# Kernel optimization log

Measured on AMD Instinct MI355X. Metric: run time of the kernel, lower is better.

Reference implementation:

```python
import jax, jax.numpy as jnp
import numpy as np

NEG_SLOPE = 0.2
EPS = 1e-16

N_NODES = 100000
N_EDGES = 1600000
CHANNELS = 128
M_LAYERS = 3


def setup_inputs() -> dict:
    key = jax.random.key(0)
    k1, k2, k3, k4, k5 = jax.random.split(key, 5)
    x = jax.random.normal(k1, (N_NODES, CHANNELS), dtype=jnp.float32)
    edge_index = jax.random.randint(k2, (2, N_EDGES), 0, N_NODES, dtype=jnp.int64)
    # Glorot-ish scaled params, stacked over layers
    Ws = jax.random.normal(k3, (M_LAYERS, CHANNELS, CHANNELS), dtype=jnp.float32) / np.sqrt(CHANNELS)
    att_src = jax.random.normal(k4, (M_LAYERS, CHANNELS), dtype=jnp.float32) / np.sqrt(CHANNELS)
    att_dst = jax.random.normal(k5, (M_LAYERS, CHANNELS), dtype=jnp.float32) / np.sqrt(CHANNELS)
    bias = jnp.zeros((M_LAYERS, CHANNELS), dtype=jnp.float32)
    return {"x": x, "edge_index": edge_index, "Ws": Ws, "att_src": att_src,
            "att_dst": att_dst, "bias": bias}


def _gat_conv(x, src, dst, W, a_src, a_dst, b, n_nodes):
    # single-head PyG GATConv (heads=1, concat) with self-loops already in src/dst
    h = x @ W                                   # [N, C]
    s = h @ a_src                               # [N] per-node source score
    d = h @ a_dst                               # [N] per-node dest score
    e = s[src] + d[dst]                         # [E]
    e = jnp.where(e > 0, e, NEG_SLOPE * e)      # LeakyReLU(0.2)
    # segment softmax over edges grouped by destination node
    e_max = jax.ops.segment_max(e, dst, num_segments=n_nodes)
    e_max = jnp.where(jnp.isfinite(e_max), e_max, 0.0)
    w = jnp.exp(e - e_max[dst])                 # [E]
    denom = jax.ops.segment_sum(w, dst, num_segments=n_nodes)
    alpha = w / (denom[dst] + EPS)              # [E]
    out = jax.ops.segment_sum(alpha[:, None] * h[src], dst, num_segments=n_nodes)
    return out + b


def reference(x, edge_index, Ws, att_src, att_dst, bias):
    n = x.shape[0]
    loop = jnp.arange(n, dtype=edge_index.dtype)
    src = jnp.concatenate([edge_index[0], loop])   # add self loops (PyG default)
    dst = jnp.concatenate([edge_index[1], loop])
    for m in range(Ws.shape[0]):
        x = x + jax.nn.sigmoid(
            _gat_conv(x, src, dst, Ws[m], att_src[m], att_dst[m], bias[m], n))
    return x
```

## Files before the change

kernel.cpp:

```cpp
#include <hip/hip_runtime.h>
#include <hip/hip_bf16.h>
#include <math.h>

#define CH 128
#define LAYERS 3
#define NEG_SLOPE 0.2f
#define EPS_D 1e-16f
#define NBUCK_MAX 512
#define BIN_CHUNK 8192
#define PAIR_STRIDE 4608

typedef __attribute__((ext_vector_type(8))) short bf16x8;
typedef __attribute__((ext_vector_type(4))) short s16x4;
typedef __attribute__((ext_vector_type(4))) float f32x4;
typedef __attribute__((ext_vector_type(2))) float f32x2;

__device__ __forceinline__ float leaky(float e) { return e > 0.f ? e : NEG_SLOPE * e; }
__device__ __forceinline__ float sigm(float x) { return 1.f / (1.f + __expf(-x)); }

__device__ __forceinline__ unsigned bf16rne(float f) {
    unsigned u = __float_as_uint(f);
    return (u + 0x7fffu + ((u >> 16) & 1u)) >> 16;
}
__device__ __forceinline__ unsigned pack2(float f0, float f1) {
    return bf16rne(f0) | (bf16rne(f1) << 16);
}

__global__ __launch_bounds__(256) void bin_k(const int* __restrict__ EI,
                                             int* __restrict__ bcursor,
                                             unsigned* __restrict__ pairs,
                                             int ne, int nbuck) {
    __shared__ int hist[NBUCK_MAX];
    __shared__ int base[NBUCK_MAX];
    const int t = threadIdx.x;
    const int e0 = blockIdx.x * BIN_CHUNK;
    const int e1 = min(e0 + BIN_CHUNK, ne);

    for (int i = t; i < nbuck; i += 256) hist[i] = 0;
    __syncthreads();
    for (int e = e0 + t; e < e1; e += 256)
        atomicAdd(&hist[EI[ne + e] >> 8], 1);
    __syncthreads();
    for (int i = t; i < nbuck; i += 256) {
        int c = hist[i];
        base[i] = (c > 0) ? (i * PAIR_STRIDE + atomicAdd(&bcursor[i], c)) : 0;
        hist[i] = 0;
    }
    __syncthreads();
    for (int e = e0 + t; e < e1; e += 256) {
        int src = EI[e], dst = EI[ne + e];
        int b = dst >> 8;
        int off = atomicAdd(&hist[b], 1);
        pairs[base[b] + off] = ((unsigned)src << 8) | (unsigned)(dst & 255);
    }
}

__global__ __launch_bounds__(256) void bscat_k(const int* __restrict__ bcursor,
                                               const unsigned* __restrict__ pairs,
                                               int* __restrict__ col,
                                               int* __restrict__ rowbeg,
                                               int* __restrict__ rowend, int n) {
    __shared__ int hist[256];
    __shared__ int cur[256];
    __shared__ int wsum[4];
    const int b = blockIdx.x;
    const int node0 = b << 8;
    const int t = threadIdx.x;
    const int lane = t & 63, w = t >> 6;

    hist[t] = 0;
    __syncthreads();
    const int pbase = b * PAIR_STRIDE;
    const int tot = bcursor[b];
    for (int i = t; i < tot; i += 256)
        atomicAdd(&hist[pairs[pbase + i] & 255u], 1);
    __syncthreads();

    int v = hist[t];
    int sc = v;
#pragma unroll
    for (int off = 1; off < 64; off <<= 1) {
        int x = __shfl_up(sc, off);
        if (lane >= off) sc += x;
    }
    if (lane == 63) wsum[w] = sc;
    __syncthreads();
    if (t == 0) {
        int a = 0;
#pragma unroll
        for (int j = 0; j < 4; j++) { int tmp = wsum[j]; wsum[j] = a; a += tmp; }
    }
    __syncthreads();
    int excl = sc - v + wsum[w];
    int node = node0 + t;
    int rp = pbase + excl;
    if (node < n) {
        rowbeg[node] = rp;
        rowend[node] = rp + v;
        cur[t] = rp;
    }
    __syncthreads();

    for (int i = t; i < tot; i += 256) {
        unsigned p = pairs[pbase + i];
        int pos = atomicAdd(&cur[p & 255u], 1);
        col[pos] = (int)(p >> 8);
    }
}

__global__ __launch_bounds__(512) void gemm_k(const float* __restrict__ X,
                                              const float* __restrict__ Wm,
                                              const float* __restrict__ asrc,
                                              const float* __restrict__ adst,
                                              unsigned* __restrict__ Hf8,
                                              float* __restrict__ s,
                                              float* __restrict__ d, int n) {
    __shared__ short WT[128 * 132];
    const int t = threadIdx.x;
    const int node0 = blockIdx.x * 128;

    unsigned* WT32 = (unsigned*)WT;
#pragma unroll
    for (int i = 0; i < 16; i++) {
        int item = i * 512 + t;
        int c = item & 127, k2 = item >> 7;
        float va = Wm[(2 * k2) * 128 + c];
        float vb = Wm[(2 * k2 + 1) * 128 + c];
        WT32[c * 66 + k2] = pack2(va, vb);
    }
    __syncthreads();

    const int lane = t & 63, w = t >> 6;
    const int lr = lane & 15, lg = lane >> 4;
    const int row = w * 16 + lr;
    const int node = node0 + row;
    const int nodeA = min(node, n - 1);
    const float* xrow = X + (size_t)nodeA * CH;

    f32x4 acc[8];
#pragma unroll
    for (int ct = 0; ct < 8; ct++) acc[ct] = (f32x4){0.f, 0.f, 0.f, 0.f};

#pragma unroll
    for (int kt = 0; kt < 4; kt++) {
        const int kb = kt * 32 + lg * 8;
        const float4 fa = *(const float4*)&xrow[kb];
        const float4 fb = *(const float4*)&xrow[kb + 4];
        bf16x8 a;
        a[0] = (short)bf16rne(fa.x); a[1] = (short)bf16rne(fa.y);
        a[2] = (short)bf16rne(fa.z); a[3] = (short)bf16rne(fa.w);
        a[4] = (short)bf16rne(fb.x); a[5] = (short)bf16rne(fb.y);
        a[6] = (short)bf16rne(fb.z); a[7] = (short)bf16rne(fb.w);
#pragma unroll
        for (int ct = 0; ct < 8; ct++) {
            const int cc = ct * 16 + lr;
            s16x4 b0 = *(s16x4*)&WT[cc * 132 + kb];
            s16x4 b1 = *(s16x4*)&WT[cc * 132 + kb + 4];
            bf16x8 bb = {b0[0], b0[1], b0[2], b0[3], b1[0], b1[1], b1[2], b1[3]};
            acc[ct] = __builtin_amdgcn_mfma_f32_16x16x32_bf16(a, bb, acc[ct], 0, 0, 0);
        }
    }

    float asv[8], adv[8];
#pragma unroll
    for (int ct = 0; ct < 8; ct++) { asv[ct] = asrc[ct * 16 + lr]; adv[ct] = adst[ct * 16 + lr]; }

#pragma unroll
    for (int r = 0; r < 4; r++) {
        const int orow = w * 16 + lg * 4 + r;
        const int onode = node0 + orow;
        float ps = 0.f, pd = 0.f;
#pragma unroll
        for (int ct = 0; ct < 8; ct++) {
            float hv = acc[ct][r];
            ps += hv * asv[ct];
            pd += hv * adv[ct];
        }
        if (onode < n) {
            int w0 = __builtin_amdgcn_cvt_pk_fp8_f32(acc[0][r], acc[1][r], 0, false);
            w0 = __builtin_amdgcn_cvt_pk_fp8_f32(acc[2][r], acc[3][r], w0, true);
            int w1 = __builtin_amdgcn_cvt_pk_fp8_f32(acc[4][r], acc[5][r], 0, false);
            w1 = __builtin_amdgcn_cvt_pk_fp8_f32(acc[6][r], acc[7][r], w1, true);
            uint2 q8; q8.x = (unsigned)w0; q8.y = (unsigned)w1;
            *(uint2*)&Hf8[(size_t)onode * 32 + lr * 2] = q8;
        }
#pragma unroll
        for (int off = 8; off >= 1; off >>= 1) {
            ps += __shfl_xor(ps, off);
            pd += __shfl_xor(pd, off);
        }
        if (lr == 0 && onode < n) { s[onode] = ps; d[onode] = pd; }
    }
}

__global__ __launch_bounds__(256) void node_aggr_k(const int* __restrict__ rowbeg,
                                                   const int* __restrict__ rowend,
                                                   const int* __restrict__ col,
                                                   const float* __restrict__ s,
                                                   const float* __restrict__ d,
                                                   const unsigned* __restrict__ Hf8,
                                                   const float* __restrict__ bias,
                                                   const float* __restrict__ x_prev,
                                                   float* __restrict__ x_next, int n) {
    long g = (long)blockIdx.x * 256 + threadIdx.x;
    int node = (int)(g >> 4);
    if (node >= n) return;
    const int tid = threadIdx.x;
    const int sub = tid & 15;
    const int qbase = tid & 48;

    const int beg = rowbeg[node], end = rowend[node];
    const float dn = d[node];
    const float ev_self = leaky(s[node] + dn);

    float m = ev_self;
    float l = 0.f;
    float o[8];
#pragma unroll
    for (int k = 0; k < 8; k++) o[k] = 0.f;

    for (int j0 = beg; j0 < end; j0 += 16) {
        int cnt = min(16, end - j0);
        int srcv = 0;
        float ev = -INFINITY;
        if (sub < cnt) {
            srcv = col[j0 + sub];
            ev = leaky(s[srcv] + dn);
        }
        float bmax = ev;
#pragma unroll
        for (int off = 8; off >= 1; off >>= 1) bmax = fmaxf(bmax, __shfl_xor(bmax, off));
        float newm = fmaxf(m, bmax);
        float scale = __expf(m - newm);
        l *= scale;
#pragma unroll
        for (int k = 0; k < 8; k++) o[k] *= scale;
        m = newm;
        float wv = (sub < cnt) ? __expf(ev - m) : 0.f;

        for (int j = 0; j < cnt; j += 4) {
            int i1 = min(j + 1, cnt - 1), i2 = min(j + 2, cnt - 1), i3 = min(j + 3, cnt - 1);
            int se0 = __shfl(srcv, qbase + j);
            int se1 = __shfl(srcv, qbase + i1);
            int se2 = __shfl(srcv, qbase + i2);
            int se3 = __shfl(srcv, qbase + i3);
            float w0 = __shfl(wv, qbase + j);
            float w1 = __shfl(wv, qbase + i1);
            float w2 = __shfl(wv, qbase + i2);
            float w3 = __shfl(wv, qbase + i3);
            w1 = (j + 1 < cnt) ? w1 : 0.f;
            w2 = (j + 2 < cnt) ? w2 : 0.f;
            w3 = (j + 3 < cnt) ? w3 : 0.f;
            const uint2 u0 = *(const uint2*)&Hf8[(size_t)se0 * 32 + sub * 2];
            const uint2 u1 = *(const uint2*)&Hf8[(size_t)se1 * 32 + sub * 2];
            const uint2 u2 = *(const uint2*)&Hf8[(size_t)se2 * 32 + sub * 2];
            const uint2 u3 = *(const uint2*)&Hf8[(size_t)se3 * 32 + sub * 2];
            l += w0 + w1 + w2 + w3;
            {
                f32x2 p0 = __builtin_amdgcn_cvt_pk_f32_fp8(u0.x, false);
                f32x2 p1 = __builtin_amdgcn_cvt_pk_f32_fp8(u0.x, true);
                f32x2 p2 = __builtin_amdgcn_cvt_pk_f32_fp8(u0.y, false);
                f32x2 p3 = __builtin_amdgcn_cvt_pk_f32_fp8(u0.y, true);
                o[0] += w0 * p0[0]; o[1] += w0 * p0[1];
                o[2] += w0 * p1[0]; o[3] += w0 * p1[1];
                o[4] += w0 * p2[0]; o[5] += w0 * p2[1];
                o[6] += w0 * p3[0]; o[7] += w0 * p3[1];
            }
            {
                f32x2 p0 = __builtin_amdgcn_cvt_pk_f32_fp8(u1.x, false);
                f32x2 p1 = __builtin_amdgcn_cvt_pk_f32_fp8(u1.x, true);
                f32x2 p2 = __builtin_amdgcn_cvt_pk_f32_fp8(u1.y, false);
                f32x2 p3 = __builtin_amdgcn_cvt_pk_f32_fp8(u1.y, true);
                o[0] += w1 * p0[0]; o[1] += w1 * p0[1];
                o[2] += w1 * p1[0]; o[3] += w1 * p1[1];
                o[4] += w1 * p2[0]; o[5] += w1 * p2[1];
                o[6] += w1 * p3[0]; o[7] += w1 * p3[1];
            }
            {
                f32x2 p0 = __builtin_amdgcn_cvt_pk_f32_fp8(u2.x, false);
                f32x2 p1 = __builtin_amdgcn_cvt_pk_f32_fp8(u2.x, true);
                f32x2 p2 = __builtin_amdgcn_cvt_pk_f32_fp8(u2.y, false);
                f32x2 p3 = __builtin_amdgcn_cvt_pk_f32_fp8(u2.y, true);
                o[0] += w2 * p0[0]; o[1] += w2 * p0[1];
                o[2] += w2 * p1[0]; o[3] += w2 * p1[1];
                o[4] += w2 * p2[0]; o[5] += w2 * p2[1];
                o[6] += w2 * p3[0]; o[7] += w2 * p3[1];
            }
            {
                f32x2 p0 = __builtin_amdgcn_cvt_pk_f32_fp8(u3.x, false);
                f32x2 p1 = __builtin_amdgcn_cvt_pk_f32_fp8(u3.x, true);
                f32x2 p2 = __builtin_amdgcn_cvt_pk_f32_fp8(u3.y, false);
                f32x2 p3 = __builtin_amdgcn_cvt_pk_f32_fp8(u3.y, true);
                o[0] += w3 * p0[0]; o[1] += w3 * p0[1];
                o[2] += w3 * p1[0]; o[3] += w3 * p1[1];
                o[4] += w3 * p2[0]; o[5] += w3 * p2[1];
                o[6] += w3 * p3[0]; o[7] += w3 * p3[1];
            }
        }
    }

    float wself = __expf(ev_self - m);
    l += wself;
    const uint2 us = *(const uint2*)&Hf8[(size_t)node * 32 + sub * 2];
    {
        f32x2 p0 = __builtin_amdgcn_cvt_pk_f32_fp8(us.x, false);
        f32x2 p1 = __builtin_amdgcn_cvt_pk_f32_fp8(us.x, true);
        f32x2 p2 = __builtin_amdgcn_cvt_pk_f32_fp8(us.y, false);
        f32x2 p3 = __builtin_amdgcn_cvt_pk_f32_fp8(us.y, true);
        o[0] += wself * p0[0]; o[1] += wself * p0[1];
        o[2] += wself * p1[0]; o[3] += wself * p1[1];
        o[4] += wself * p2[0]; o[5] += wself * p2[1];
        o[6] += wself * p3[0]; o[7] += wself * p3[1];
    }

    float inv = 1.f / (l + EPS_D);
    const long rowb = (long)node * CH;
#pragma unroll
    for (int k = 0; k < 8; k++) {
        int c = k * 16 + sub;
        float r = x_prev[rowb + c] + sigm(o[k] * inv + bias[c]);
        x_next[rowb + c] = r;
    }
}

extern "C" void kernel_launch(void* const* d_in, const int* in_sizes, int n_in,
                              void* d_out, int out_size, void* d_ws, size_t ws_size,
                              hipStream_t stream) {
    const float* x_in = (const float*)d_in[0];
    const int* EI = (const int*)d_in[1];
    const float* Ws_all = (const float*)d_in[2];
    const float* asrc_all = (const float*)d_in[3];
    const float* adst_all = (const float*)d_in[4];
    const float* bias_all = (const float*)d_in[5];
    float* out = (float*)d_out;

    const int n = in_sizes[0] / CH;
    const int ne = in_sizes[1] / 2;
    const long NC = (long)n * CH;
    const int nbuck = (n + 255) >> 8;

    unsigned* hf8 = (unsigned*)d_ws;
    float* s = (float*)(hf8 + NC / 4);
    float* dd = s + n;
    float* x_ws = dd + n;
    int* rowbeg = (int*)(x_ws + NC);
    int* rowend = rowbeg + n;
    int* bcursor = rowend + n;
    int* colv = bcursor + nbuck;
    unsigned* pairs = (unsigned*)(colv + nbuck * PAIR_STRIDE);

    hipMemsetAsync(bcursor, 0, (size_t)nbuck * sizeof(int), stream);
    bin_k<<<(ne + BIN_CHUNK - 1) / BIN_CHUNK, 256, 0, stream>>>(EI, bcursor, pairs, ne, nbuck);
    bscat_k<<<nbuck, 256, 0, stream>>>(bcursor, pairs, colv, rowbeg, rowend, n);

    const float* xp[LAYERS] = {x_in, out, x_ws};
    float* xn[LAYERS] = {out, x_ws, out};

    for (int m = 0; m < LAYERS; m++) {
        const float* Wm = Ws_all + (size_t)m * CH * CH;
        const float* as = asrc_all + (size_t)m * CH;
        const float* ad = adst_all + (size_t)m * CH;
        const float* bm = bias_all + (size_t)m * CH;

        gemm_k<<<(n + 127) / 128, 512, 0, stream>>>(xp[m], Wm, as, ad, hf8, s, dd, n);
        node_aggr_k<<<((long)n * 16 + 255) / 256, 256, 0, stream>>>(rowbeg, rowend, colv,
                                                                    s, dd, hf8, bm,
                                                                    xp[m], xn[m], n);
    }
}
```

Measured before the change: 241.9 us.

## Store intermediate layer activations in bf16 and use packed f32x2 accumulation

Intermediate residual activations between layers are now written and read as bf16 rather than fp32, which halves that traffic in the gemm and aggregation kernels. The gemm can then load bf16 rows directly with no per-element conversion. The aggregation accumulator is rewritten to use f32x2 vectors so the compiler can emit packed FMA instructions. The cost is extra rounding error in the residual stream, which carries across layers.

```diff
diff --git a/kernel.cpp b/kernel.cpp
--- a/kernel.cpp
+++ b/kernel.cpp
@@ -24,6 +24,9 @@
 }
 __device__ __forceinline__ unsigned pack2(float f0, float f1) {
     return bf16rne(f0) | (bf16rne(f1) << 16);
+}
+__device__ __forceinline__ float bf16tof(unsigned short v) {
+    return __uint_as_float(((unsigned)v) << 16);
 }
 
 __global__ __launch_bounds__(256) void bin_k(const int* __restrict__ EI,
@@ -108,7 +111,8 @@
     }
 }
 
-__global__ __launch_bounds__(512) void gemm_k(const float* __restrict__ X,
+template <int XBF16>
+__global__ __launch_bounds__(512) void gemm_k(const void* __restrict__ Xv,
                                               const float* __restrict__ Wm,
                                               const float* __restrict__ asrc,
                                               const float* __restrict__ adst,
@@ -135,7 +139,6 @@
     const int row = w * 16 + lr;
     const int node = node0 + row;
     const int nodeA = min(node, n - 1);
-    const float* xrow = X + (size_t)nodeA * CH;
 
     f32x4 acc[8];
 #pragma unroll
@@ -144,13 +147,19 @@
 #pragma unroll
     for (int kt = 0; kt < 4; kt++) {
         const int kb = kt * 32 + lg * 8;
-        const float4 fa = *(const float4*)&xrow[kb];
-        const float4 fb = *(const float4*)&xrow[kb + 4];
         bf16x8 a;
-        a[0] = (short)bf16rne(fa.x); a[1] = (short)bf16rne(fa.y);
-        a[2] = (short)bf16rne(fa.z); a[3] = (short)bf16rne(fa.w);
-        a[4] = (short)bf16rne(fb.x); a[5] = (short)bf16rne(fb.y);
-        a[6] = (short)bf16rne(fb.z); a[7] = (short)bf16rne(fb.w);
+        if (XBF16) {
+            const unsigned short* xrow = (const unsigned short*)Xv + (size_t)nodeA * CH;
+            a = *(const bf16x8*)&xrow[kb];
+        } else {
+            const float* xrow = (const float*)Xv + (size_t)nodeA * CH;
+            const float4 fa = *(const float4*)&xrow[kb];
+            const float4 fb = *(const float4*)&xrow[kb + 4];
+            a[0] = (short)bf16rne(fa.x); a[1] = (short)bf16rne(fa.y);
+            a[2] = (short)bf16rne(fa.z); a[3] = (short)bf16rne(fa.w);
+            a[4] = (short)bf16rne(fb.x); a[5] = (short)bf16rne(fb.y);
+            a[6] = (short)bf16rne(fb.z); a[7] = (short)bf16rne(fb.w);
+        }
 #pragma unroll
         for (int ct = 0; ct < 8; ct++) {
             const int cc = ct * 16 + lr;
@@ -193,6 +202,15 @@
     }
 }
 
+__device__ __forceinline__ void acc_edge(f32x2* o2, const uint2 u, float we) {
+    f32x2 w2 = {we, we};
+    o2[0] += w2 * __builtin_amdgcn_cvt_pk_f32_fp8(u.x, false);
+    o2[1] += w2 * __builtin_amdgcn_cvt_pk_f32_fp8(u.x, true);
+    o2[2] += w2 * __builtin_amdgcn_cvt_pk_f32_fp8(u.y, false);
+    o2[3] += w2 * __builtin_amdgcn_cvt_pk_f32_fp8(u.y, true);
+}
+
+template <int PBF16, int NBF16>
 __global__ __launch_bounds__(256) void node_aggr_k(const int* __restrict__ rowbeg,
                                                    const int* __restrict__ rowend,
                                                    const int* __restrict__ col,
@@ -200,8 +218,8 @@
                                                    const float* __restrict__ d,
                                                    const unsigned* __restrict__ Hf8,
                                                    const float* __restrict__ bias,
-                                                   const float* __restrict__ x_prev,
-                                                   float* __restrict__ x_next, int n) {
+                                                   const void* __restrict__ x_prev,
+                                                   void* __restrict__ x_next, int n) {
     long g = (long)blockIdx.x * 256 + threadIdx.x;
     int node = (int)(g >> 4);
     if (node >= n) return;
@@ -215,9 +233,9 @@
 
     float m = ev_self;
     float l = 0.f;
-    float o[8];
-#pragma unroll
-    for (int k = 0; k < 8; k++) o[k] = 0.f;
+    f32x2 o2[4];
+#pragma unroll
+    for (int j = 0; j < 4; j++) o2[j] = (f32x2){0.f, 0.f};
 
     for (int j0 = beg; j0 < end; j0 += 16) {
         int cnt = min(16, end - j0);
@@ -232,9 +250,10 @@
         for (int off = 8; off >= 1; off >>= 1) bmax = fmaxf(bmax, __shfl_xor(bmax, off));
         float newm = fmaxf(m, bmax);
         float scale = __expf(m - newm);
+        f32x2 sc2 = {scale, scale};
         l *= scale;
 #pragma unroll
-        for (int k = 0; k < 8; k++) o[k] *= scale;
+        for (int j = 0; j < 4; j++) o2[j] *= sc2;
         m = newm;
         float wv = (sub < cnt) ? __expf(ev - m) : 0.f;
 
@@ -256,70 +275,31 @@
             const uint2 u2 = *(const uint2*)&Hf8[(size_t)se2 * 32 + sub * 2];
             const uint2 u3 = *(const uint2*)&Hf8[(size_t)se3 * 32 + sub * 2];
             l += w0 + w1 + w2 + w3;
-            {
-                f32x2 p0 = __builtin_amdgcn_cvt_pk_f32_fp8(u0.x, false);
-                f32x2 p1 = __builtin_amdgcn_cvt_pk_f32_fp8(u0.x, true);
-                f32x2 p2 = __builtin_amdgcn_cvt_pk_f32_fp8(u0.y, false);
-                f32x2 p3 = __builtin_amdgcn_cvt_pk_f32_fp8(u0.y, true);
-                o[0] += w0 * p0[0]; o[1] += w0 * p0[1];
-                o[2] += w0 * p1[0]; o[3] += w0 * p1[1];
-                o[4] += w0 * p2[0]; o[5] += w0 * p2[1];
-                o[6] += w0 * p3[0]; o[7] += w0 * p3[1];
-            }
-            {
-                f32x2 p0 = __builtin_amdgcn_cvt_pk_f32_fp8(u1.x, false);
-                f32x2 p1 = __builtin_amdgcn_cvt_pk_f32_fp8(u1.x, true);
-                f32x2 p2 = __builtin_amdgcn_cvt_pk_f32_fp8(u1.y, false);
-                f32x2 p3 = __builtin_amdgcn_cvt_pk_f32_fp8(u1.y, true);
-                o[0] += w1 * p0[0]; o[1] += w1 * p0[1];
-                o[2] += w1 * p1[0]; o[3] += w1 * p1[1];
-                o[4] += w1 * p2[0]; o[5] += w1 * p2[1];
-                o[6] += w1 * p3[0]; o[7] += w1 * p3[1];
-            }
-            {
-                f32x2 p0 = __builtin_amdgcn_cvt_pk_f32_fp8(u2.x, false);
-                f32x2 p1 = __builtin_amdgcn_cvt_pk_f32_fp8(u2.x, true);
-                f32x2 p2 = __builtin_amdgcn_cvt_pk_f32_fp8(u2.y, false);
-                f32x2 p3 = __builtin_amdgcn_cvt_pk_f32_fp8(u2.y, true);
-                o[0] += w2 * p0[0]; o[1] += w2 * p0[1];
-                o[2] += w2 * p1[0]; o[3] += w2 * p1[1];
-                o[4] += w2 * p2[0]; o[5] += w2 * p2[1];
-                o[6] += w2 * p3[0]; o[7] += w2 * p3[1];
-            }
-            {
-                f32x2 p0 = __builtin_amdgcn_cvt_pk_f32_fp8(u3.x, false);
-                f32x2 p1 = __builtin_amdgcn_cvt_pk_f32_fp8(u3.x, true);
-                f32x2 p2 = __builtin_amdgcn_cvt_pk_f32_fp8(u3.y, false);
-                f32x2 p3 = __builtin_amdgcn_cvt_pk_f32_fp8(u3.y, true);
-                o[0] += w3 * p0[0]; o[1] += w3 * p0[1];
-                o[2] += w3 * p1[0]; o[3] += w3 * p1[1];
-                o[4] += w3 * p2[0]; o[5] += w3 * p2[1];
-                o[6] += w3 * p3[0]; o[7] += w3 * p3[1];
-            }
+            acc_edge(o2, u0, w0);
+            acc_edge(o2, u1, w1);
+            acc_edge(o2, u2, w2);
+            acc_edge(o2, u3, w3);
         }
     }
 
     float wself = __expf(ev_self - m);
     l += wself;
     const uint2 us = *(const uint2*)&Hf8[(size_t)node * 32 + sub * 2];
-    {
-        f32x2 p0 = __builtin_amdgcn_cvt_pk_f32_fp8(us.x, false);
-        f32x2 p1 = __builtin_amdgcn_cvt_pk_f32_fp8(us.x, true);
-        f32x2 p2 = __builtin_amdgcn_cvt_pk_f32_fp8(us.y, false);
-        f32x2 p3 = __builtin_amdgcn_cvt_pk_f32_fp8(us.y, true);
-        o[0] += wself * p0[0]; o[1] += wself * p0[1];
-        o[2] += wself * p1[0]; o[3] += wself * p1[1];
-        o[4] += wself * p2[0]; o[5] += wself * p2[1];
-        o[6] += wself * p3[0]; o[7] += wself * p3[1];
-    }
+    acc_edge(o2, us, wself);
 
     float inv = 1.f / (l + EPS_D);
     const long rowb = (long)node * CH;
 #pragma unroll
     for (int k = 0; k < 8; k++) {
         int c = k * 16 + sub;
-        float r = x_prev[rowb + c] + sigm(o[k] * inv + bias[c]);
-        x_next[rowb + c] = r;
+        float ov = o2[k >> 1][k & 1];
+        float xv = PBF16 ? bf16tof(((const unsigned short*)x_prev)[rowb + c])
+                         : ((const float*)x_prev)[rowb + c];
+        float r = xv + sigm(ov * inv + bias[c]);
+        if (NBF16)
+            ((unsigned short*)x_next)[rowb + c] = (unsigned short)bf16rne(r);
+        else
+            ((float*)x_next)[rowb + c] = r;
     }
 }
 
@@ -342,8 +322,9 @@
     unsigned* hf8 = (unsigned*)d_ws;
     float* s = (float*)(hf8 + NC / 4);
     float* dd = s + n;
-    float* x_ws = dd + n;
-    int* rowbeg = (int*)(x_ws + NC);
+    unsigned short* xb0 = (unsigned short*)(dd + n);
+    unsigned short* xb1 = xb0 + NC;
+    int* rowbeg = (int*)(xb1 + NC);
     int* rowend = rowbeg + n;
     int* bcursor = rowend + n;
     int* colv = bcursor + nbuck;
@@ -353,18 +334,26 @@
     bin_k<<<(ne + BIN_CHUNK - 1) / BIN_CHUNK, 256, 0, stream>>>(EI, bcursor, pairs, ne, nbuck);
     bscat_k<<<nbuck, 256, 0, stream>>>(bcursor, pairs, colv, rowbeg, rowend, n);
 
-    const float* xp[LAYERS] = {x_in, out, x_ws};
-    float* xn[LAYERS] = {out, x_ws, out};
-
-    for (int m = 0; m < LAYERS; m++) {
-        const float* Wm = Ws_all + (size_t)m * CH * CH;
-        const float* as = asrc_all + (size_t)m * CH;
-        const float* ad = adst_all + (size_t)m * CH;
-        const float* bm = bias_all + (size_t)m * CH;
-
-        gemm_k<<<(n + 127) / 128, 512, 0, stream>>>(xp[m], Wm, as, ad, hf8, s, dd, n);
-        node_aggr_k<<<((long)n * 16 + 255) / 256, 256, 0, stream>>>(rowbeg, rowend, colv,
-                                                                    s, dd, hf8, bm,
-                                                                    xp[m], xn[m], n);
-    }
-}
+    const int gG = (n + 127) / 128;
+    const int gA = (int)(((long)n * 16 + 255) / 256);
+
+    {
+        const float* Wm = Ws_all;
+        gemm_k<0><<<gG, 512, 0, stream>>>(x_in, Wm, asrc_all, adst_all, hf8, s, dd, n);
+        node_aggr_k<0, 1><<<gA, 256, 0, stream>>>(rowbeg, rowend, colv, s, dd, hf8,
+                                                  bias_all, x_in, xb0, n);
+    }
+    {
+        const float* Wm = Ws_all + (size_t)1 * CH * CH;
+        gemm_k<1><<<gG, 512, 0, stream>>>(xb0, Wm, asrc_all + CH, adst_all + CH, hf8, s, dd, n);
+        node_aggr_k<1, 1><<<gA, 256, 0, stream>>>(rowbeg, rowend, colv, s, dd, hf8,
+                                                  bias_all + CH, xb0, xb1, n);
+    }
+    {
+        const float* Wm = Ws_all + (size_t)2 * CH * CH;
+        gemm_k<1><<<gG, 512, 0, stream>>>(xb1, Wm, asrc_all + 2 * CH, adst_all + 2 * CH,
+                                          hf8, s, dd, n);
+        node_aggr_k<1, 0><<<gA, 256, 0, stream>>>(rowbeg, rowend, colv, s, dd, hf8,
+                                                  bias_all + 2 * CH, xb1, out, n);
+    }
+}
```

Result: faster. 222.6 us (-8.0%).
